# Optimization experiments

Hardware: AMD Instinct MI355X
Metric: run time of the kernel (lower is better)

Reference implementation:

```python
import jax, jax.numpy as jnp
import numpy as np

DIMS = 64
D_MODEL = 1024

def setup_inputs() -> dict:
    key = jax.random.key(0)
    ks = jax.random.split(key, 8)
    B, Sk, Sq = 4, 4096, 2048
    enc = jax.random.normal(ks[0], (B, Sk, D_MODEL), dtype=jnp.float32)
    dec = jax.random.normal(ks[1], (B, Sq, D_MODEL), dtype=jnp.float32)
    s = 1.0 / np.sqrt(D_MODEL)
    Wq = jax.random.normal(ks[2], (D_MODEL, DIMS), dtype=jnp.float32) * s
    Wk = jax.random.normal(ks[3], (D_MODEL, DIMS), dtype=jnp.float32) * s
    Wv = jax.random.normal(ks[4], (D_MODEL, DIMS), dtype=jnp.float32) * s
    bq = jnp.zeros((DIMS,), jnp.float32)
    bk = jnp.zeros((DIMS,), jnp.float32)
    bv = jnp.zeros((DIMS,), jnp.float32)
    return {"encoder_output": enc, "decoder": dec, "Wq": Wq, "bq": bq,
            "Wk": Wk, "bk": bk, "Wv": Wv, "bv": bv}

def reference(encoder_output, decoder, Wq, bq, Wk, bk, Wv, bv):
    # q: [B,Sq,dims], k/v: [B,Sk,dims]
    q = decoder @ Wq + bq
    k = encoder_output @ Wk + bk
    v = encoder_output @ Wv + bv
    scale = DIMS ** (-0.5)
    scores = jnp.einsum('bqd,bkd->bqk', q, k) * scale  # [B,Sq,Sk]
    attn = jax.nn.softmax(scores, axis=-1)
    out = jnp.einsum('bqk,bkd->bqd', attn, v)  # [B,Sq,dims]
    return out
```

## Files before the change

kernel.cpp:

```cpp
#include <hip/hip_runtime.h>
#include <hip/hip_bf16.h>

typedef __attribute__((ext_vector_type(8))) short short8;
typedef __attribute__((ext_vector_type(4))) float f32x4;
typedef unsigned short u16;

__device__ __forceinline__ u16 f2bf(float x) {
    union { float f; unsigned u; } v; v.f = x;
    return (u16)((v.u + 0x7FFFu + ((v.u >> 16) & 1u)) >> 16);
}

__device__ __forceinline__ void gl_lds16(const void* g, void* l) {
    __builtin_amdgcn_global_load_lds(
        (const __attribute__((address_space(1))) unsigned int*)g,
        (__attribute__((address_space(3))) unsigned int*)l, 16, 0, 0);
}

#define WTQ_OFF   0
#define WTKV_OFF  131072
#define Q_OFF     393216
#define K_OFF     1441792
#define VT_OFF    3538944
#define OPART_OFF 5636096
#define MPART_OFF 14024704
#define LPART_OFF 14155776

__global__ __launch_bounds__(256) void prep2(
    const float* __restrict__ Wq, const float* __restrict__ Wk,
    const float* __restrict__ Wv, u16* __restrict__ wtq, u16* __restrict__ wtkv)
{
    __shared__ u16 tile[64][66];
    const int t = threadIdx.x;
    const int mat = blockIdx.x >> 4, kc = blockIdx.x & 15;
    const float* src = (mat == 0) ? Wq : ((mat == 1) ? Wk : Wv);
    u16* dst = (mat == 0) ? wtq : (wtkv + ((mat == 2) ? 64 * 1024 : 0));
    #pragma unroll
    for (int c = 0; c < 4; ++c) {
        int id = t + c * 256;
        int r = id >> 4, c4 = id & 15;
        float4 v = *(const float4*)(src + (size_t)(kc * 64 + r) * 64 + c4 * 4);
        tile[r][c4 * 4 + 0] = f2bf(v.x);
        tile[r][c4 * 4 + 1] = f2bf(v.y);
        tile[r][c4 * 4 + 2] = f2bf(v.z);
        tile[r][c4 * 4 + 3] = f2bf(v.w);
    }
    __syncthreads();
    int n = t >> 2, kch = t & 3;
    short8 v0, v1;
    #pragma unroll
    for (int j = 0; j < 8; ++j) {
        v0[j] = (short)tile[kch * 16 + j][n];
        v1[j] = (short)tile[kch * 16 + 8 + j][n];
    }
    u16* dp = dst + (size_t)n * 1024 + kc * 64 + kch * 16;
    *(short8*)dp = v0;
    *(short8*)(dp + 8) = v1;
}

template<int NOUT>
__global__ __launch_bounds__(256) void proj2(
    const float* __restrict__ A, const u16* __restrict__ Wt,
    const float* __restrict__ bias0, const float* __restrict__ bias1,
    u16* __restrict__ out0, u16* __restrict__ outT, float scale)
{
    constexpr int NREP = NOUT / 32;
    constexpr int WCH = NOUT / 32;
    constexpr int ABYTES = 64 * 64 * 4;
    constexpr int WBYTES = NOUT * 64 * 2;
    constexpr int BUF = ABYTES + WBYTES;
    __shared__ __align__(16) char lds[2 * BUF];

    const int t = threadIdx.x, l = t & 63, w = t >> 6;
    const int wm = w >> 1, wn = w & 1;
    const int r0 = blockIdx.x * 64;

    f32x4 acc[2][NREP];
    #pragma unroll
    for (int m = 0; m < 2; ++m)
        #pragma unroll
        for (int n = 0; n < NREP; ++n)
            acc[m][n] = (f32x4){0.f, 0.f, 0.f, 0.f};

    auto stage = [&](int buf, int kt) {
        char* Ab = lds + buf * BUF;
        char* Wb = Ab + ABYTES;
        const int k0 = kt * 64;
        #pragma unroll
        for (int c = 0; c < 4; ++c) {
            int id = t + c * 256;
            int row = id >> 4, sl = id & 15;
            int k4 = sl ^ (row & 7);
            gl_lds16(A + (size_t)(r0 + row) * 1024 + k0 + k4 * 4, Ab + id * 16);
        }
        #pragma unroll
        for (int c = 0; c < WCH; ++c) {
            int id = t + c * 256;
            int row = id >> 3, sl = id & 7;
            int c8 = sl ^ (row & 7);
            gl_lds16(Wt + (size_t)row * 1024 + k0 + c8 * 8, Wb + id * 16);
        }
    };

    stage(0, 0);
    __syncthreads();
    int cur = 0;
    for (int kt = 0; kt < 16; ++kt) {
        if (kt < 15) stage(cur ^ 1, kt + 1);
        const char* Ab = lds + cur * BUF;
        const char* Wb = Ab + ABYTES;
        #pragma unroll
        for (int ks = 0; ks < 2; ++ks) {
            short8 afr[2], bfr[NREP];
            #pragma unroll
            for (int m = 0; m < 2; ++m) {
                int row = wm * 32 + m * 16 + (l & 15);
                int s0 = ks * 8 + (l >> 4) * 2;
                f32x4 lo = *(const f32x4*)(Ab + row * 256 + ((s0 ^ (row & 7)) << 4));
                f32x4 hi = *(const f32x4*)(Ab + row * 256 + (((s0 + 1) ^ (row & 7)) << 4));
                short8 r;
                r[0] = (short)f2bf(lo[0]); r[1] = (short)f2bf(lo[1]);
                r[2] = (short)f2bf(lo[2]); r[3] = (short)f2bf(lo[3]);
                r[4] = (short)f2bf(hi[0]); r[5] = (short)f2bf(hi[1]);
                r[6] = (short)f2bf(hi[2]); r[7] = (short)f2bf(hi[3]);
                afr[m] = r;
            }
            #pragma unroll
            for (int n = 0; n < NREP; ++n) {
                int row = wn * (NOUT / 2) + n * 16 + (l & 15);
                int c8 = ks * 4 + (l >> 4);
                bfr[n] = *(const short8*)(Wb + row * 128 + ((c8 ^ (row & 7)) << 4));
            }
            #pragma unroll
            for (int m = 0; m < 2; ++m)
                #pragma unroll
                for (int n = 0; n < NREP; ++n)
                    acc[m][n] = __builtin_amdgcn_mfma_f32_16x16x32_bf16(
                        afr[m], bfr[n], acc[m][n], 0, 0, 0);
        }
        __syncthreads();
        cur ^= 1;
    }

    u16* Vs2 = (u16*)lds;
    #pragma unroll
    for (int m = 0; m < 2; ++m) {
        #pragma unroll
        for (int n = 0; n < NREP; ++n) {
            int col = wn * (NOUT / 2) + n * 16 + (l & 15);
            #pragma unroll
            for (int i = 0; i < 4; ++i) {
                int lrow = wm * 32 + m * 16 + (l >> 4) * 4 + i;
                if (NOUT == 64 || wn == 0) {
                    float val = (acc[m][n][i] + bias0[col]) * scale;
                    out0[(size_t)(r0 + lrow) * 64 + col] = f2bf(val);
                } else {
                    int d = col - 64;
                    float val = (acc[m][n][i] + bias1[d]) * scale;
                    Vs2[lrow * 66 + d] = f2bf(val);
                }
            }
        }
    }
    if (NOUT == 128) {
        __syncthreads();
        int d = t >> 2, sch = t & 3;
        short8 v0, v1;
        #pragma unroll
        for (int j = 0; j < 8; ++j) {
            v0[j] = (short)Vs2[(sch * 16 + j) * 66 + d];
            v1[j] = (short)Vs2[(sch * 16 + 8 + j) * 66 + d];
        }
        int b = r0 >> 12, s0 = r0 & 4095;
        u16* dp = outT + (((size_t)(b * 64 + d)) << 12) + s0 + sch * 16;
        *(short8*)dp = v0;
        *(short8*)(dp + 8) = v1;
    }
}

__global__ __launch_bounds__(256) void attn_kernel(
    const u16* __restrict__ Qb, const u16* __restrict__ Kb,
    const u16* __restrict__ Vtb, float* __restrict__ Opart,
    float* __restrict__ Mpart, float* __restrict__ Lpart)
{
    __shared__ __align__(16) char lds[36864];
    const int t = threadIdx.x;
    const int l = t & 63, w = t >> 6;
    const int b = blockIdx.y, bz = blockIdx.z;
    const int q0 = blockIdx.x * 32;

    char* Ks = lds + w * 9216;
    char* Vs = Ks + 4096;
    char* Ps = Ks;

    short8 qf[2][2];
    #pragma unroll
    for (int m = 0; m < 2; ++m)
        #pragma unroll
        for (int ks = 0; ks < 2; ++ks)
            qf[m][ks] = *(const short8*)(Qb
                + (size_t)(b * 2048 + q0 + m * 16 + (l & 15)) * 64
                + ks * 32 + (l >> 4) * 8);

    f32x4 o[2][4];
    #pragma unroll
    for (int m = 0; m < 2; ++m)
        #pragma unroll
        for (int n = 0; n < 4; ++n)
            o[m][n] = (f32x4){0.f, 0.f, 0.f, 0.f};
    float m_run[2][4], l_run[2][4];
    #pragma unroll
    for (int m = 0; m < 2; ++m)
        #pragma unroll
        for (int i = 0; i < 4; ++i) { m_run[m][i] = -INFINITY; l_run[m][i] = 0.f; }

    const size_t kbase = (size_t)b * 4096 * 64;
    const size_t vbase = (size_t)b * 64 * 4096;
    const int kt0 = bz * 1024 + w * 256;

    for (int tile = 0; tile < 8; ++tile) {
        const int kt = kt0 + tile * 32;
        #pragma unroll
        for (int c = 0; c < 4; ++c) {
            int id = c * 64 + l;
            int key = id >> 3, sl = id & 7;
            int c8 = sl ^ (key & 7);
            gl_lds16(Kb + kbase + (size_t)(kt + key) * 64 + c8 * 8, Ks + id * 16);
        }
        #pragma unroll
        for (int c = 0; c < 4; ++c) {
            int ci = c * 64 + l;
            int d = ci >> 2, kc = ci & 3;
            short8 v = *(const short8*)(Vtb + vbase + (size_t)d * 4096 + kt + kc * 8);
            *(short8*)(Vs + d * 80 + kc * 16) = v;
        }
        asm volatile("s_waitcnt vmcnt(0)" ::: "memory");
        f32x4 s[2][2];
        #pragma unroll
        for (int m = 0; m < 2; ++m)
            #pragma unroll
            for (int n = 0; n < 2; ++n)
                s[m][n] = (f32x4){0.f, 0.f, 0.f, 0.f};
        #pragma unroll
        for (int ks = 0; ks < 2; ++ks) {
            int sl8 = ks * 4 + (l >> 4);
            #pragma unroll
            for (int n = 0; n < 2; ++n) {
                int kr = n * 16 + (l & 15);
                short8 kf = *(const short8*)(Ks + kr * 128 + ((sl8 ^ (kr & 7)) << 4));
                #pragma unroll
                for (int m = 0; m < 2; ++m)
                    s[m][n] = __builtin_amdgcn_mfma_f32_16x16x32_bf16(
                        qf[m][ks], kf, s[m][n], 0, 0, 0);
            }
        }
        #pragma unroll
        for (int m = 0; m < 2; ++m) {
            #pragma unroll
            for (int i = 0; i < 4; ++i) {
                float pm = fmaxf(s[m][0][i], s[m][1][i]);
                pm = fmaxf(pm, __shfl_xor(pm, 1));
                pm = fmaxf(pm, __shfl_xor(pm, 2));
                pm = fmaxf(pm, __shfl_xor(pm, 4));
                pm = fmaxf(pm, __shfl_xor(pm, 8));
                float mo = m_run[m][i];
                float mn = fmaxf(mo, pm);
                m_run[m][i] = mn;
                float corr = __expf(mo - mn);
                float p0 = __expf(s[m][0][i] - mn);
                float p1 = __expf(s[m][1][i] - mn);
                float rs = p0 + p1;
                rs += __shfl_xor(rs, 1);
                rs += __shfl_xor(rs, 2);
                rs += __shfl_xor(rs, 4);
                rs += __shfl_xor(rs, 8);
                l_run[m][i] = l_run[m][i] * corr + rs;
                #pragma unroll
                for (int n = 0; n < 4; ++n) o[m][n][i] *= corr;
                int prow = m * 16 + (l >> 4) * 4 + i;
                *(u16*)(Ps + prow * 80 + (l & 15) * 2) = f2bf(p0);
                *(u16*)(Ps + prow * 80 + 32 + (l & 15) * 2) = f2bf(p1);
            }
        }
        #pragma unroll
        for (int m = 0; m < 2; ++m) {
            int prow = m * 16 + (l & 15);
            short8 pa = *(const short8*)(Ps + prow * 80 + (l >> 4) * 16);
            #pragma unroll
            for (int n = 0; n < 4; ++n) {
                int vr = n * 16 + (l & 15);
                short8 vf = *(const short8*)(Vs + vr * 80 + (l >> 4) * 16);
                o[m][n] = __builtin_amdgcn_mfma_f32_16x16x32_bf16(pa, vf, o[m][n], 0, 0, 0);
            }
        }
    }

    __syncthreads();
    float* Oc = (float*)lds;
    float* ml = (float*)(lds + 32768);
    #pragma unroll
    for (int m = 0; m < 2; ++m)
        #pragma unroll
        for (int n = 0; n < 4; ++n)
            #pragma unroll
            for (int i = 0; i < 4; ++i) {
                int row = m * 16 + (l >> 4) * 4 + i;
                int d = n * 16 + (l & 15);
                Oc[(w * 32 + row) * 64 + d] = o[m][n][i];
            }
    if ((l & 15) == 0) {
        #pragma unroll
        for (int m = 0; m < 2; ++m)
            #pragma unroll
            for (int i = 0; i < 4; ++i) {
                int row = m * 16 + (l >> 4) * 4 + i;
                ml[w * 64 + row] = m_run[m][i];
                ml[w * 64 + 32 + row] = l_run[m][i];
            }
    }
    __syncthreads();
    {
        int row = t >> 3, dc = (t & 7) * 8;
        float mw[4], M = -INFINITY;
        #pragma unroll
        for (int ww = 0; ww < 4; ++ww) { mw[ww] = ml[ww * 64 + row]; M = fmaxf(M, mw[ww]); }
        float sc4[4], L = 0.f;
        #pragma unroll
        for (int ww = 0; ww < 4; ++ww) {
            sc4[ww] = __expf(mw[ww] - M);
            L += ml[ww * 64 + 32 + row] * sc4[ww];
        }
        float vals[8];
        #pragma unroll
        for (int j = 0; j < 8; ++j) {
            float a = 0.f;
            #pragma unroll
            for (int ww = 0; ww < 4; ++ww)
                a += Oc[(ww * 32 + row) * 64 + dc + j] * sc4[ww];
            vals[j] = a;
        }
        size_t gq = (size_t)b * 2048 + q0 + row;
        float* op = Opart + ((size_t)bz * 8192 + gq) * 64 + dc;
        *(float4*)op = make_float4(vals[0], vals[1], vals[2], vals[3]);
        *(float4*)(op + 4) = make_float4(vals[4], vals[5], vals[6], vals[7]);
        if ((t & 7) == 0) {
            Mpart[bz * 8192 + gq] = M;
            Lpart[bz * 8192 + gq] = L;
        }
    }
}

__global__ __launch_bounds__(256) void attn_combine(
    const float* __restrict__ Opart, const float* __restrict__ Mpart,
    const float* __restrict__ Lpart, float* __restrict__ Out)
{
    int idx = blockIdx.x * 256 + threadIdx.x;
    int row = idx >> 3, dc = (idx & 7) * 8;
    float mv[4], M = -INFINITY;
    #pragma unroll
    for (int ks = 0; ks < 4; ++ks) { mv[ks] = Mpart[ks * 8192 + row]; M = fmaxf(M, mv[ks]); }
    float wk[4], L = 0.f;
    #pragma unroll
    for (int ks = 0; ks < 4; ++ks) {
        wk[ks] = __expf(mv[ks] - M);
        L += Lpart[ks * 8192 + row] * wk[ks];
    }
    float inv = 1.0f / L;
    float o[8] = {0.f, 0.f, 0.f, 0.f, 0.f, 0.f, 0.f, 0.f};
    #pragma unroll
    for (int ks = 0; ks < 4; ++ks) {
        const float* p = Opart + ((size_t)ks * 8192 + row) * 64 + dc;
        float4 a = *(const float4*)p;
        float4 bb = *(const float4*)(p + 4);
        o[0] += a.x * wk[ks]; o[1] += a.y * wk[ks];
        o[2] += a.z * wk[ks]; o[3] += a.w * wk[ks];
        o[4] += bb.x * wk[ks]; o[5] += bb.y * wk[ks];
        o[6] += bb.z * wk[ks]; o[7] += bb.w * wk[ks];
    }
    float* dst = Out + (size_t)row * 64 + dc;
    *(float4*)dst = make_float4(o[0] * inv, o[1] * inv, o[2] * inv, o[3] * inv);
    *(float4*)(dst + 4) = make_float4(o[4] * inv, o[5] * inv, o[6] * inv, o[7] * inv);
}

extern "C" void kernel_launch(void* const* d_in, const int* in_sizes, int n_in,
                              void* d_out, int out_size, void* d_ws, size_t ws_size,
                              hipStream_t stream) {
    const float* enc = (const float*)d_in[0];
    const float* dec = (const float*)d_in[1];
    const float* Wq  = (const float*)d_in[2];
    const float* bq  = (const float*)d_in[3];
    const float* Wk  = (const float*)d_in[4];
    const float* bk  = (const float*)d_in[5];
    const float* Wv  = (const float*)d_in[6];
    const float* bv  = (const float*)d_in[7];

    char* ws = (char*)d_ws;
    u16* wtq    = (u16*)(ws + WTQ_OFF);
    u16* wtkv   = (u16*)(ws + WTKV_OFF);
    u16* Qb     = (u16*)(ws + Q_OFF);
    u16* Kb     = (u16*)(ws + K_OFF);
    u16* Vtb    = (u16*)(ws + VT_OFF);
    float* Opart = (float*)(ws + OPART_OFF);
    float* Mpart = (float*)(ws + MPART_OFF);
    float* Lpart = (float*)(ws + LPART_OFF);

    prep2<<<48, 256, 0, stream>>>(Wq, Wk, Wv, wtq, wtkv);
    proj2<128><<<256, 256, 0, stream>>>(enc, wtkv, bk, bv, Kb, Vtb, 1.0f);
    proj2<64><<<128, 256, 0, stream>>>(dec, wtq, bq, bq, Qb, (u16*)nullptr, 0.125f);
    attn_kernel<<<dim3(64, 4, 4), 256, 0, stream>>>(Qb, Kb, Vtb, Opart, Mpart, Lpart);
    attn_combine<<<256, 256, 0, stream>>>(Opart, Mpart, Lpart, (float*)d_out);
}
```

Before: 204.3 us.

## Rewrite attention with 32x32 MFMA register pipeline, fused projections, 8-way key split

Replaces the attention kernel with a per-wave 32-query design that uses 32x32x16 bf16 MFMAs, holds K/V fragments in registers with double-buffered global loads instead of LDS staging, and builds the P operand with packed bf16 conversion plus permlane32 swaps. The two projection launches are merged into one 768-block kernel with smaller row tiles. The key dimension is split 8 ways when the workspace allows, with a transposed partial-output layout and a new combine kernel that transposes through LDS. Softmax moves to exp2 with a log2e factor. The aim is to cut LDS traffic and shuffle reductions and to raise parallelism, at the cost of more register pressure and more partial-output traffic.

After: 179.7 us. -12.0%, faster.

```diff
diff --git a/kernel.cpp b/kernel.cpp
--- a/kernel.cpp
+++ b/kernel.cpp
@@ -3,7 +3,10 @@
 
 typedef __attribute__((ext_vector_type(8))) short short8;
 typedef __attribute__((ext_vector_type(4))) float f32x4;
+typedef __attribute__((ext_vector_type(16))) float f32x16;
 typedef unsigned short u16;
+
+#define L2E 1.4426950408889634f
 
 __device__ __forceinline__ u16 f2bf(float x) {
     union { float f; unsigned u; } v; v.f = x;
@@ -14,6 +17,16 @@
     __builtin_amdgcn_global_load_lds(
         (const __attribute__((address_space(1))) unsigned int*)g,
         (__attribute__((address_space(3))) unsigned int*)l, 16, 0, 0);
+}
+
+__device__ __forceinline__ int cvtpk(float lo, float hi) {
+    int r;
+    asm("v_cvt_pk_bf16_f32 %0, %1, %2" : "=v"(r) : "v"(lo), "v"(hi));
+    return r;
+}
+
+__device__ __forceinline__ void plswap(int& a, int& b) {
+    asm volatile("v_permlane32_swap_b32 %0, %1" : "+v"(a), "+v"(b));
 }
 
 #define WTQ_OFF   0
@@ -21,9 +34,7 @@
 #define Q_OFF     393216
 #define K_OFF     1441792
 #define VT_OFF    3538944
-#define OPART_OFF 5636096
-#define MPART_OFF 14024704
-#define LPART_OFF 14155776
+#define OPT_OFF   5636096
 
 __global__ __launch_bounds__(256) void prep2(
     const float* __restrict__ Wq, const float* __restrict__ Wk,
@@ -57,47 +68,47 @@
     *(short8*)(dp + 8) = v1;
 }
 
-template<int NOUT>
-__global__ __launch_bounds__(256) void proj2(
-    const float* __restrict__ A, const u16* __restrict__ Wt,
-    const float* __restrict__ bias0, const float* __restrict__ bias1,
-    u16* __restrict__ out0, u16* __restrict__ outT, float scale)
+__global__ __launch_bounds__(256) void proj3(
+    const float* __restrict__ enc, const float* __restrict__ dec,
+    const u16* __restrict__ wtkv, const u16* __restrict__ wtq,
+    const float* __restrict__ bk, const float* __restrict__ bv,
+    const float* __restrict__ bq,
+    u16* __restrict__ Kb, u16* __restrict__ Vtb, u16* __restrict__ Qb)
 {
-    constexpr int NREP = NOUT / 32;
-    constexpr int WCH = NOUT / 32;
-    constexpr int ABYTES = 64 * 64 * 4;
-    constexpr int WBYTES = NOUT * 64 * 2;
+    constexpr int ABYTES = 32 * 64 * 4;
+    constexpr int WBYTES = 128 * 64 * 2;
     constexpr int BUF = ABYTES + WBYTES;
     __shared__ __align__(16) char lds[2 * BUF];
 
     const int t = threadIdx.x, l = t & 63, w = t >> 6;
     const int wm = w >> 1, wn = w & 1;
-    const int r0 = blockIdx.x * 64;
-
-    f32x4 acc[2][NREP];
-    #pragma unroll
-    for (int m = 0; m < 2; ++m)
-        #pragma unroll
-        for (int n = 0; n < NREP; ++n)
-            acc[m][n] = (f32x4){0.f, 0.f, 0.f, 0.f};
+    const bool is_enc = blockIdx.x < 512;
+    const int r0 = is_enc ? blockIdx.x * 32 : (blockIdx.x - 512) * 32;
+    const float* A = is_enc ? enc : dec;
+    const u16* Wsrc = is_enc ? wtkv : wtq;
+
+    f32x4 acc[4];
+    #pragma unroll
+    for (int n = 0; n < 4; ++n) acc[n] = (f32x4){0.f, 0.f, 0.f, 0.f};
 
     auto stage = [&](int buf, int kt) {
         char* Ab = lds + buf * BUF;
         char* Wb = Ab + ABYTES;
         const int k0 = kt * 64;
         #pragma unroll
+        for (int c = 0; c < 2; ++c) {
+            int id = t + c * 256;
+            int row = id >> 4, sl = id & 15;
+            gl_lds16(A + (size_t)(r0 + row) * 1024 + k0 + ((sl ^ (row & 7)) << 2),
+                     Ab + id * 16);
+        }
+        #pragma unroll
         for (int c = 0; c < 4; ++c) {
             int id = t + c * 256;
-            int row = id >> 4, sl = id & 15;
-            int k4 = sl ^ (row & 7);
-            gl_lds16(A + (size_t)(r0 + row) * 1024 + k0 + k4 * 4, Ab + id * 16);
-        }
-        #pragma unroll
-        for (int c = 0; c < WCH; ++c) {
-            int id = t + c * 256;
             int row = id >> 3, sl = id & 7;
-            int c8 = sl ^ (row & 7);
-            gl_lds16(Wt + (size_t)row * 1024 + k0 + c8 * 8, Wb + id * 16);
+            int wr = is_enc ? row : (row & 63);
+            gl_lds16(Wsrc + (size_t)wr * 1024 + k0 + ((sl ^ (row & 7)) << 3),
+                     Wb + id * 16);
         }
     };
 
@@ -110,275 +121,242 @@
         const char* Wb = Ab + ABYTES;
         #pragma unroll
         for (int ks = 0; ks < 2; ++ks) {
-            short8 afr[2], bfr[NREP];
-            #pragma unroll
-            for (int m = 0; m < 2; ++m) {
-                int row = wm * 32 + m * 16 + (l & 15);
-                int s0 = ks * 8 + (l >> 4) * 2;
-                f32x4 lo = *(const f32x4*)(Ab + row * 256 + ((s0 ^ (row & 7)) << 4));
-                f32x4 hi = *(const f32x4*)(Ab + row * 256 + (((s0 + 1) ^ (row & 7)) << 4));
-                short8 r;
-                r[0] = (short)f2bf(lo[0]); r[1] = (short)f2bf(lo[1]);
-                r[2] = (short)f2bf(lo[2]); r[3] = (short)f2bf(lo[3]);
-                r[4] = (short)f2bf(hi[0]); r[5] = (short)f2bf(hi[1]);
-                r[6] = (short)f2bf(hi[2]); r[7] = (short)f2bf(hi[3]);
-                afr[m] = r;
-            }
-            #pragma unroll
-            for (int n = 0; n < NREP; ++n) {
-                int row = wn * (NOUT / 2) + n * 16 + (l & 15);
+            int arow = wm * 16 + (l & 15);
+            int s0 = ks * 8 + (l >> 4) * 2;
+            f32x4 lo = *(const f32x4*)(Ab + arow * 256 + ((s0 ^ (arow & 7)) << 4));
+            f32x4 hi = *(const f32x4*)(Ab + arow * 256 + (((s0 + 1) ^ (arow & 7)) << 4));
+            short8 afr;
+            afr[0] = (short)f2bf(lo[0]); afr[1] = (short)f2bf(lo[1]);
+            afr[2] = (short)f2bf(lo[2]); afr[3] = (short)f2bf(lo[3]);
+            afr[4] = (short)f2bf(hi[0]); afr[5] = (short)f2bf(hi[1]);
+            afr[6] = (short)f2bf(hi[2]); afr[7] = (short)f2bf(hi[3]);
+            #pragma unroll
+            for (int n = 0; n < 4; ++n) {
+                int wrow = wn * 64 + n * 16 + (l & 15);
                 int c8 = ks * 4 + (l >> 4);
-                bfr[n] = *(const short8*)(Wb + row * 128 + ((c8 ^ (row & 7)) << 4));
-            }
-            #pragma unroll
-            for (int m = 0; m < 2; ++m)
-                #pragma unroll
-                for (int n = 0; n < NREP; ++n)
-                    acc[m][n] = __builtin_amdgcn_mfma_f32_16x16x32_bf16(
-                        afr[m], bfr[n], acc[m][n], 0, 0, 0);
+                short8 bfr = *(const short8*)(Wb + wrow * 128 + ((c8 ^ (wrow & 7)) << 4));
+                acc[n] = __builtin_amdgcn_mfma_f32_16x16x32_bf16(afr, bfr, acc[n], 0, 0, 0);
+            }
         }
         __syncthreads();
         cur ^= 1;
     }
 
     u16* Vs2 = (u16*)lds;
-    #pragma unroll
-    for (int m = 0; m < 2; ++m) {
-        #pragma unroll
-        for (int n = 0; n < NREP; ++n) {
-            int col = wn * (NOUT / 2) + n * 16 + (l & 15);
-            #pragma unroll
-            for (int i = 0; i < 4; ++i) {
-                int lrow = wm * 32 + m * 16 + (l >> 4) * 4 + i;
-                if (NOUT == 64 || wn == 0) {
-                    float val = (acc[m][n][i] + bias0[col]) * scale;
-                    out0[(size_t)(r0 + lrow) * 64 + col] = f2bf(val);
-                } else {
-                    int d = col - 64;
-                    float val = (acc[m][n][i] + bias1[d]) * scale;
-                    Vs2[lrow * 66 + d] = f2bf(val);
+    if (is_enc) {
+        if (wn == 0) {
+            #pragma unroll
+            for (int n = 0; n < 4; ++n) {
+                int col = n * 16 + (l & 15);
+                #pragma unroll
+                for (int i = 0; i < 4; ++i) {
+                    int lrow = wm * 16 + (l >> 4) * 4 + i;
+                    Kb[(size_t)(r0 + lrow) * 64 + col] = f2bf(acc[n][i] + bk[col]);
                 }
             }
-        }
-    }
-    if (NOUT == 128) {
+        } else {
+            #pragma unroll
+            for (int n = 0; n < 4; ++n) {
+                int d = n * 16 + (l & 15);
+                #pragma unroll
+                for (int i = 0; i < 4; ++i) {
+                    int lrow = wm * 16 + (l >> 4) * 4 + i;
+                    Vs2[lrow * 66 + d] = f2bf(acc[n][i] + bv[d]);
+                }
+            }
+        }
         __syncthreads();
         int d = t >> 2, sch = t & 3;
-        short8 v0, v1;
-        #pragma unroll
-        for (int j = 0; j < 8; ++j) {
-            v0[j] = (short)Vs2[(sch * 16 + j) * 66 + d];
-            v1[j] = (short)Vs2[(sch * 16 + 8 + j) * 66 + d];
-        }
-        int b = r0 >> 12, s0 = r0 & 4095;
-        u16* dp = outT + (((size_t)(b * 64 + d)) << 12) + s0 + sch * 16;
-        *(short8*)dp = v0;
-        *(short8*)(dp + 8) = v1;
-    }
-}
-
-__global__ __launch_bounds__(256) void attn_kernel(
+        short8 v;
+        #pragma unroll
+        for (int j = 0; j < 8; ++j) v[j] = (short)Vs2[(sch * 8 + j) * 66 + d];
+        int bb = r0 >> 12, s0r = r0 & 4095;
+        *(short8*)(Vtb + ((size_t)(bb * 64 + d)) * 4096 + s0r + sch * 8) = v;
+    } else {
+        if (wn == 0) {
+            #pragma unroll
+            for (int n = 0; n < 4; ++n) {
+                int col = n * 16 + (l & 15);
+                #pragma unroll
+                for (int i = 0; i < 4; ++i) {
+                    int lrow = wm * 16 + (l >> 4) * 4 + i;
+                    Qb[(size_t)(r0 + lrow) * 64 + col] =
+                        f2bf((acc[n][i] + bq[col]) * 0.125f);
+                }
+            }
+        }
+    }
+}
+
+template<int NS>
+__global__ __launch_bounds__(256, 2) void attn3(
     const u16* __restrict__ Qb, const u16* __restrict__ Kb,
-    const u16* __restrict__ Vtb, float* __restrict__ Opart,
+    const u16* __restrict__ Vtb, float* __restrict__ OpT,
     float* __restrict__ Mpart, float* __restrict__ Lpart)
 {
-    __shared__ __align__(16) char lds[36864];
-    const int t = threadIdx.x;
-    const int l = t & 63, w = t >> 6;
+    constexpr int SPAN = 4096 / NS;
+    constexpr int NIT = SPAN / 64;
+    const int t = threadIdx.x, l = t & 63, w = t >> 6;
     const int b = blockIdx.y, bz = blockIdx.z;
-    const int q0 = blockIdx.x * 32;
-
-    char* Ks = lds + w * 9216;
-    char* Vs = Ks + 4096;
-    char* Ps = Ks;
-
-    short8 qf[2][2];
-    #pragma unroll
-    for (int m = 0; m < 2; ++m)
-        #pragma unroll
-        for (int ks = 0; ks < 2; ++ks)
-            qf[m][ks] = *(const short8*)(Qb
-                + (size_t)(b * 2048 + q0 + m * 16 + (l & 15)) * 64
-                + ks * 32 + (l >> 4) * 8);
-
-    f32x4 o[2][4];
-    #pragma unroll
-    for (int m = 0; m < 2; ++m)
-        #pragma unroll
-        for (int n = 0; n < 4; ++n)
-            o[m][n] = (f32x4){0.f, 0.f, 0.f, 0.f};
-    float m_run[2][4], l_run[2][4];
-    #pragma unroll
-    for (int m = 0; m < 2; ++m)
-        #pragma unroll
-        for (int i = 0; i < 4; ++i) { m_run[m][i] = -INFINITY; l_run[m][i] = 0.f; }
+    const int q0 = (blockIdx.x * 4 + w) * 32;
+    const int lq = l & 31, lh = l >> 5;
+
+    short8 qf[4];
+    #pragma unroll
+    for (int dt = 0; dt < 4; ++dt)
+        qf[dt] = *(const short8*)(Qb + (size_t)(b * 2048 + q0 + lq) * 64
+                                  + dt * 16 + lh * 8);
+
+    f32x16 o0, o1;
+    #pragma unroll
+    for (int r = 0; r < 16; ++r) { o0[r] = 0.f; o1[r] = 0.f; }
+    float mrun = -INFINITY, lrun = 0.f;
 
     const size_t kbase = (size_t)b * 4096 * 64;
     const size_t vbase = (size_t)b * 64 * 4096;
-    const int kt0 = bz * 1024 + w * 256;
-
-    for (int tile = 0; tile < 8; ++tile) {
-        const int kt = kt0 + tile * 32;
-        #pragma unroll
-        for (int c = 0; c < 4; ++c) {
-            int id = c * 64 + l;
-            int key = id >> 3, sl = id & 7;
-            int c8 = sl ^ (key & 7);
-            gl_lds16(Kb + kbase + (size_t)(kt + key) * 64 + c8 * 8, Ks + id * 16);
-        }
-        #pragma unroll
-        for (int c = 0; c < 4; ++c) {
-            int ci = c * 64 + l;
-            int d = ci >> 2, kc = ci & 3;
-            short8 v = *(const short8*)(Vtb + vbase + (size_t)d * 4096 + kt + kc * 8);
-            *(short8*)(Vs + d * 80 + kc * 16) = v;
-        }
-        asm volatile("s_waitcnt vmcnt(0)" ::: "memory");
-        f32x4 s[2][2];
-        #pragma unroll
-        for (int m = 0; m < 2; ++m)
-            #pragma unroll
-            for (int n = 0; n < 2; ++n)
-                s[m][n] = (f32x4){0.f, 0.f, 0.f, 0.f};
-        #pragma unroll
-        for (int ks = 0; ks < 2; ++ks) {
-            int sl8 = ks * 4 + (l >> 4);
-            #pragma unroll
-            for (int n = 0; n < 2; ++n) {
-                int kr = n * 16 + (l & 15);
-                short8 kf = *(const short8*)(Ks + kr * 128 + ((sl8 ^ (kr & 7)) << 4));
-                #pragma unroll
-                for (int m = 0; m < 2; ++m)
-                    s[m][n] = __builtin_amdgcn_mfma_f32_16x16x32_bf16(
-                        qf[m][ks], kf, s[m][n], 0, 0, 0);
-            }
-        }
-        #pragma unroll
-        for (int m = 0; m < 2; ++m) {
-            #pragma unroll
-            for (int i = 0; i < 4; ++i) {
-                float pm = fmaxf(s[m][0][i], s[m][1][i]);
-                pm = fmaxf(pm, __shfl_xor(pm, 1));
-                pm = fmaxf(pm, __shfl_xor(pm, 2));
-                pm = fmaxf(pm, __shfl_xor(pm, 4));
-                pm = fmaxf(pm, __shfl_xor(pm, 8));
-                float mo = m_run[m][i];
-                float mn = fmaxf(mo, pm);
-                m_run[m][i] = mn;
-                float corr = __expf(mo - mn);
-                float p0 = __expf(s[m][0][i] - mn);
-                float p1 = __expf(s[m][1][i] - mn);
-                float rs = p0 + p1;
-                rs += __shfl_xor(rs, 1);
-                rs += __shfl_xor(rs, 2);
-                rs += __shfl_xor(rs, 4);
-                rs += __shfl_xor(rs, 8);
-                l_run[m][i] = l_run[m][i] * corr + rs;
-                #pragma unroll
-                for (int n = 0; n < 4; ++n) o[m][n][i] *= corr;
-                int prow = m * 16 + (l >> 4) * 4 + i;
-                *(u16*)(Ps + prow * 80 + (l & 15) * 2) = f2bf(p0);
-                *(u16*)(Ps + prow * 80 + 32 + (l & 15) * 2) = f2bf(p1);
-            }
-        }
-        #pragma unroll
-        for (int m = 0; m < 2; ++m) {
-            int prow = m * 16 + (l & 15);
-            short8 pa = *(const short8*)(Ps + prow * 80 + (l >> 4) * 16);
-            #pragma unroll
-            for (int n = 0; n < 4; ++n) {
-                int vr = n * 16 + (l & 15);
-                short8 vf = *(const short8*)(Vs + vr * 80 + (l >> 4) * 16);
-                o[m][n] = __builtin_amdgcn_mfma_f32_16x16x32_bf16(pa, vf, o[m][n], 0, 0, 0);
-            }
-        }
-    }
-
-    __syncthreads();
-    float* Oc = (float*)lds;
-    float* ml = (float*)(lds + 32768);
-    #pragma unroll
-    for (int m = 0; m < 2; ++m)
-        #pragma unroll
-        for (int n = 0; n < 4; ++n)
-            #pragma unroll
-            for (int i = 0; i < 4; ++i) {
-                int row = m * 16 + (l >> 4) * 4 + i;
-                int d = n * 16 + (l & 15);
-                Oc[(w * 32 + row) * 64 + d] = o[m][n][i];
-            }
-    if ((l & 15) == 0) {
-        #pragma unroll
-        for (int m = 0; m < 2; ++m)
-            #pragma unroll
-            for (int i = 0; i < 4; ++i) {
-                int row = m * 16 + (l >> 4) * 4 + i;
-                ml[w * 64 + row] = m_run[m][i];
-                ml[w * 64 + 32 + row] = l_run[m][i];
-            }
+
+    auto LOADT = [&](short8 (&kf)[4], short8 (&vf)[2][2], int kt) {
+        #pragma unroll
+        for (int dt = 0; dt < 4; ++dt)
+            kf[dt] = *(const short8*)(Kb + kbase + (size_t)(kt + lq) * 64
+                                      + dt * 16 + lh * 8);
+        #pragma unroll
+        for (int db = 0; db < 2; ++db)
+            #pragma unroll
+            for (int kh = 0; kh < 2; ++kh)
+                vf[db][kh] = *(const short8*)(Vtb + vbase
+                                              + (size_t)(db * 32 + lq) * 4096
+                                              + kt + kh * 16 + lh * 8);
+    };
+
+    auto COMPUTE = [&](short8 (&kf)[4], short8 (&vf)[2][2]) {
+        f32x16 s;
+        #pragma unroll
+        for (int r = 0; r < 16; ++r) s[r] = 0.f;
+        #pragma unroll
+        for (int dt = 0; dt < 4; ++dt)
+            s = __builtin_amdgcn_mfma_f32_32x32x16_bf16(kf[dt], qf[dt], s, 0, 0, 0);
+        float m0 = fmaxf(fmaxf(s[0], s[1]), fmaxf(s[2], s[3]));
+        float m1 = fmaxf(fmaxf(s[4], s[5]), fmaxf(s[6], s[7]));
+        float m2 = fmaxf(fmaxf(s[8], s[9]), fmaxf(s[10], s[11]));
+        float m3 = fmaxf(fmaxf(s[12], s[13]), fmaxf(s[14], s[15]));
+        float pm = fmaxf(fmaxf(m0, m1), fmaxf(m2, m3));
+        pm = fmaxf(pm, __shfl_xor(pm, 32));
+        float mn = fmaxf(mrun, pm);
+        float corr = exp2f((mrun - mn) * L2E);
+        mrun = mn;
+        float nm = -mn * L2E;
+        float p[16];
+        #pragma unroll
+        for (int r = 0; r < 16; ++r) p[r] = exp2f(fmaf(s[r], L2E, nm));
+        float rs = ((p[0] + p[1]) + (p[2] + p[3])) + ((p[4] + p[5]) + (p[6] + p[7]))
+                 + ((p[8] + p[9]) + (p[10] + p[11])) + ((p[12] + p[13]) + (p[14] + p[15]));
+        rs += __shfl_xor(rs, 32);
+        lrun = lrun * corr + rs;
+        o0 *= corr;
+        o1 *= corr;
+        short8 pb[2];
+        #pragma unroll
+        for (int kh = 0; kh < 2; ++kh) {
+            int a0 = cvtpk(p[kh * 8 + 0], p[kh * 8 + 1]);
+            int b0 = cvtpk(p[kh * 8 + 4], p[kh * 8 + 5]);
+            int a1 = cvtpk(p[kh * 8 + 2], p[kh * 8 + 3]);
+            int b1 = cvtpk(p[kh * 8 + 6], p[kh * 8 + 7]);
+            plswap(a0, b0);
+            plswap(a1, b1);
+            union { int wd[4]; short8 v; } u;
+            u.wd[0] = a0; u.wd[1] = a1; u.wd[2] = b0; u.wd[3] = b1;
+            pb[kh] = u.v;
+        }
+        #pragma unroll
+        for (int kh = 0; kh < 2; ++kh) {
+            o0 = __builtin_amdgcn_mfma_f32_32x32x16_bf16(vf[0][kh], pb[kh], o0, 0, 0, 0);
+            o1 = __builtin_amdgcn_mfma_f32_32x32x16_bf16(vf[1][kh], pb[kh], o1, 0, 0, 0);
+        }
+    };
+
+    short8 kfA[4], vfA[2][2], kfB[4], vfB[2][2];
+    const int kt0 = bz * SPAN;
+    LOADT(kfA, vfA, kt0);
+    for (int it = 0; it < NIT; ++it) {
+        const int kt = kt0 + it * 64;
+        LOADT(kfB, vfB, kt + 32);
+        COMPUTE(kfA, vfA);
+        if (it < NIT - 1) LOADT(kfA, vfA, kt + 64);
+        COMPUTE(kfB, vfB);
+    }
+
+    const size_t obase = ((size_t)(bz * 4 + b) * 64) * 2048 + q0 + lq;
+    #pragma unroll
+    for (int r = 0; r < 16; ++r) {
+        int drow = (r & 3) + 8 * (r >> 2) + 4 * lh;
+        OpT[obase + (size_t)drow * 2048] = o0[r];
+        OpT[obase + (size_t)(drow + 32) * 2048] = o1[r];
+    }
+    if (l < 32) {
+        Mpart[bz * 8192 + b * 2048 + q0 + l] = mrun;
+        Lpart[bz * 8192 + b * 2048 + q0 + l] = lrun;
+    }
+}
+
+template<int NS>
+__global__ __launch_bounds__(256) void combine3(
+    const float* __restrict__ OpT, const float* __restrict__ Mpart,
+    const float* __restrict__ Lpart, float* __restrict__ Out)
+{
+    __shared__ float wsh[NS][32];
+    __shared__ float trans[32][72];
+    const int t = threadIdx.x;
+    const int b = blockIdx.x >> 6;
+    const int q0 = (blockIdx.x & 63) * 32;
+
+    if (t < 32) {
+        int q = t;
+        float m4[NS], M = -INFINITY;
+        #pragma unroll
+        for (int ks = 0; ks < NS; ++ks) {
+            m4[ks] = Mpart[ks * 8192 + b * 2048 + q0 + q];
+            M = fmaxf(M, m4[ks]);
+        }
+        float wv[NS], Lf = 0.f;
+        #pragma unroll
+        for (int ks = 0; ks < NS; ++ks) {
+            wv[ks] = exp2f((m4[ks] - M) * L2E);
+            Lf += Lpart[ks * 8192 + b * 2048 + q0 + q] * wv[ks];
+        }
+        float inv = 1.0f / Lf;
+        #pragma unroll
+        for (int ks = 0; ks < NS; ++ks) wsh[ks][q] = wv[ks] * inv;
     }
     __syncthreads();
     {
-        int row = t >> 3, dc = (t & 7) * 8;
-        float mw[4], M = -INFINITY;
-        #pragma unroll
-        for (int ww = 0; ww < 4; ++ww) { mw[ww] = ml[ww * 64 + row]; M = fmaxf(M, mw[ww]); }
-        float sc4[4], L = 0.f;
-        #pragma unroll
-        for (int ww = 0; ww < 4; ++ww) {
-            sc4[ww] = __expf(mw[ww] - M);
-            L += ml[ww * 64 + 32 + row] * sc4[ww];
-        }
-        float vals[8];
-        #pragma unroll
-        for (int j = 0; j < 8; ++j) {
-            float a = 0.f;
-            #pragma unroll
-            for (int ww = 0; ww < 4; ++ww)
-                a += Oc[(ww * 32 + row) * 64 + dc + j] * sc4[ww];
-            vals[j] = a;
-        }
-        size_t gq = (size_t)b * 2048 + q0 + row;
-        float* op = Opart + ((size_t)bz * 8192 + gq) * 64 + dc;
-        *(float4*)op = make_float4(vals[0], vals[1], vals[2], vals[3]);
-        *(float4*)(op + 4) = make_float4(vals[4], vals[5], vals[6], vals[7]);
-        if ((t & 7) == 0) {
-            Mpart[bz * 8192 + gq] = M;
-            Lpart[bz * 8192 + gq] = L;
-        }
-    }
-}
-
-__global__ __launch_bounds__(256) void attn_combine(
-    const float* __restrict__ Opart, const float* __restrict__ Mpart,
-    const float* __restrict__ Lpart, float* __restrict__ Out)
-{
-    int idx = blockIdx.x * 256 + threadIdx.x;
-    int row = idx >> 3, dc = (idx & 7) * 8;
-    float mv[4], M = -INFINITY;
-    #pragma unroll
-    for (int ks = 0; ks < 4; ++ks) { mv[ks] = Mpart[ks * 8192 + row]; M = fmaxf(M, mv[ks]); }
-    float wk[4], L = 0.f;
-    #pragma unroll
-    for (int ks = 0; ks < 4; ++ks) {
-        wk[ks] = __expf(mv[ks] - M);
-        L += Lpart[ks * 8192 + row] * wk[ks];
-    }
-    float inv = 1.0f / L;
-    float o[8] = {0.f, 0.f, 0.f, 0.f, 0.f, 0.f, 0.f, 0.f};
-    #pragma unroll
-    for (int ks = 0; ks < 4; ++ks) {
-        const float* p = Opart + ((size_t)ks * 8192 + row) * 64 + dc;
-        float4 a = *(const float4*)p;
-        float4 bb = *(const float4*)(p + 4);
-        o[0] += a.x * wk[ks]; o[1] += a.y * wk[ks];
-        o[2] += a.z * wk[ks]; o[3] += a.w * wk[ks];
-        o[4] += bb.x * wk[ks]; o[5] += bb.y * wk[ks];
-        o[6] += bb.z * wk[ks]; o[7] += bb.w * wk[ks];
-    }
-    float* dst = Out + (size_t)row * 64 + dc;
-    *(float4*)dst = make_float4(o[0] * inv, o[1] * inv, o[2] * inv, o[3] * inv);
-    *(float4*)(dst + 4) = make_float4(o[4] * inv, o[5] * inv, o[6] * inv, o[7] * inv);
+        int d = t >> 2, qc = (t & 3) * 8;
+        float a8[8];
+        #pragma unroll
+        for (int j = 0; j < 8; ++j) a8[j] = 0.f;
+        #pragma unroll
+        for (int ks = 0; ks < NS; ++ks) {
+            const float* p = OpT + (((size_t)(ks * 4 + b)) * 64 + d) * 2048 + q0 + qc;
+            f32x4 x = *(const f32x4*)p;
+            f32x4 y = *(const f32x4*)(p + 4);
+            #pragma unroll
+            for (int j = 0; j < 4; ++j) {
+                a8[j]     += x[j] * wsh[ks][qc + j];
+                a8[4 + j] += y[j] * wsh[ks][qc + 4 + j];
+            }
+        }
+        #pragma unroll
+        for (int j = 0; j < 8; ++j) trans[qc + j][d] = a8[j];
+    }
+    __syncthreads();
+    {
+        int q = t >> 3, dc = (t & 7) * 8;
+        f32x4 x = *(const f32x4*)&trans[q][dc];
+        f32x4 y = *(const f32x4*)&trans[q][dc + 4];
+        float* dst = Out + ((size_t)(b * 2048 + q0 + q)) * 64 + dc;
+        *(f32x4*)dst = x;
+        *(f32x4*)(dst + 4) = y;
+    }
 }
 
 extern "C" void kernel_launch(void* const* d_in, const int* in_sizes, int n_in,
@@ -394,18 +372,26 @@
     const float* bv  = (const float*)d_in[7];
 
     char* ws = (char*)d_ws;
-    u16* wtq    = (u16*)(ws + WTQ_OFF);
-    u16* wtkv   = (u16*)(ws + WTKV_OFF);
-    u16* Qb     = (u16*)(ws + Q_OFF);
-    u16* Kb     = (u16*)(ws + K_OFF);
-    u16* Vtb    = (u16*)(ws + VT_OFF);
-    float* Opart = (float*)(ws + OPART_OFF);
-    float* Mpart = (float*)(ws + MPART_OFF);
-    float* Lpart = (float*)(ws + LPART_OFF);
+    u16* wtq   = (u16*)(ws + WTQ_OFF);
+    u16* wtkv  = (u16*)(ws + WTKV_OFF);
+    u16* Qb    = (u16*)(ws + Q_OFF);
+    u16* Kb    = (u16*)(ws + K_OFF);
+    u16* Vtb   = (u16*)(ws + VT_OFF);
+    float* OpT = (float*)(ws + OPT_OFF);
 
     prep2<<<48, 256, 0, stream>>>(Wq, Wk, Wv, wtq, wtkv);
-    proj2<128><<<256, 256, 0, stream>>>(enc, wtkv, bk, bv, Kb, Vtb, 1.0f);
-    proj2<64><<<128, 256, 0, stream>>>(dec, wtq, bq, bq, Qb, (u16*)nullptr, 0.125f);
-    attn_kernel<<<dim3(64, 4, 4), 256, 0, stream>>>(Qb, Kb, Vtb, Opart, Mpart, Lpart);
-    attn_combine<<<256, 256, 0, stream>>>(Opart, Mpart, Lpart, (float*)d_out);
-}
+    proj3<<<768, 256, 0, stream>>>(enc, dec, wtkv, wtq, bk, bv, bq, Kb, Vtb, Qb);
+
+    const size_t need8 = (size_t)OPT_OFF + 8ull * 4 * 64 * 2048 * 4 + 2ull * 8 * 8192 * 4;
+    if (ws_size >= need8) {
+        float* Mpart = (float*)(ws + OPT_OFF + 8ull * 4 * 64 * 2048 * 4);
+        float* Lpart = Mpart + 8 * 8192;
+        attn3<8><<<dim3(16, 4, 8), 256, 0, stream>>>(Qb, Kb, Vtb, OpT, Mpart, Lpart);
+        combine3<8><<<256, 256, 0, stream>>>(OpT, Mpart, Lpart, (float*)d_out);
+    } else {
+        float* Mpart = (float*)(ws + OPT_OFF + 4ull * 4 * 64 * 2048 * 4);
+        float* Lpart = Mpart + 4 * 8192;
+        attn3<4><<<dim3(16, 4, 4), 256, 0, stream>>>(Qb, Kb, Vtb, OpT, Mpart, Lpart);
+        combine3<4><<<256, 256, 0, stream>>>(OpT, Mpart, Lpart, (float*)d_out);
+    }
+}
```
